# Optimization experiments

Hardware: AMD Instinct MI355X
Metric: run time of the kernel (lower is better)

The kernel has to match this reference:

```python
import jax, jax.numpy as jnp
import numpy as np


def setup_inputs() -> dict:
    key = jax.random.key(0)
    k1, k2 = jax.random.split(key)
    B, Sx, Sy, D = 8, 2048, 2048, 1024
    x = jax.random.normal(k1, (B, Sx, D), dtype=jnp.float32)
    y = jax.random.normal(k2, (B, Sy, D), dtype=jnp.float32)
    return {"x": x, "y": y}


def reference(x, y):
    # e[b,i,j] = x[b,i,:] . y[b,j,:]  (UNscaled, as in the original)
    e = jnp.einsum('bid,bjd->bij', x, y)
    ai = jax.nn.softmax(e, axis=-1)
    # a[b,i,:] = sum_j ai[b,i,j] * y[b,j,:]
    a = jnp.einsum('bij,bjd->bid', ai, y)
    # concat along feature dim; dropout p=0 -> identity
    out = jnp.concatenate([x, a], axis=-1)  # [B, Sx, 2D]
    return out
```

## Files before the change

### kernel.cpp

```cpp
#include <hip/hip_runtime.h>
#include <stdint.h>

#define SX 2048
#define SYY 2048
#define DDIM 1024
#define NBATCH 8

typedef _Float16 f16;
typedef __attribute__((ext_vector_type(2))) _Float16 h2_t;
typedef __attribute__((ext_vector_type(4))) _Float16 h4_t;
typedef __attribute__((ext_vector_type(8))) _Float16 h8_t;
typedef __attribute__((ext_vector_type(4))) float fx4_t;

__device__ __forceinline__ void gload_lds16(const void* g, void* l) {
  __builtin_amdgcn_global_load_lds((const __attribute__((address_space(1))) void*)g,
                                   (__attribute__((address_space(3))) void*)l,
                                   16, 0, 0);
}

__global__ __launch_bounds__(256) void k_prep_x(const float4* __restrict__ x,
                                                float* __restrict__ out,
                                                h4_t* __restrict__ x16, long n4) {
  long i = (long)blockIdx.x * blockDim.x + threadIdx.x;
  long stride = (long)gridDim.x * blockDim.x;
  for (; i < n4; i += stride) {
    long bi = i >> 8;
    int dq = (int)(i & 255);
    float4 v = x[i];
    *(float4*)(out + bi * (2 * DDIM) + dq * 4) = v;
    h4_t h = { (f16)v.x, (f16)v.y, (f16)v.z, (f16)v.w };
    x16[i] = h;
  }
}

__global__ __launch_bounds__(256) void k_trans(const float* __restrict__ y,
                                               f16* __restrict__ y16,
                                               f16* __restrict__ yt16) {
  __shared__ f16 tile[64][72];
  int z = blockIdx.z;
  int d0 = blockIdx.x * 64, j0 = blockIdx.y * 64;
  const float* yb = y + (size_t)z * SYY * DDIM;
  f16* y16b = y16 + (size_t)z * SYY * DDIM;
  f16* ytb = yt16 + (size_t)z * DDIM * SYY;
  int t = threadIdx.x;
  int jl = t >> 2;
  int dq = t & 3;
#pragma unroll
  for (int s = 0; s < 4; ++s) {
    int dl = dq * 16 + s * 4;
    float4 v = *(const float4*)(yb + (size_t)(j0 + jl) * DDIM + d0 + dl);
    h4_t h = { (f16)v.x, (f16)v.y, (f16)v.z, (f16)v.w };
    *(h4_t*)(y16b + (size_t)(j0 + jl) * DDIM + d0 + dl) = h;
    *(h4_t*)&tile[jl][dl] = h;
  }
  __syncthreads();
  int dl2 = t >> 2;
  int jq = t & 3;
  f16 vbuf[16] __attribute__((aligned(16)));
#pragma unroll
  for (int u = 0; u < 16; ++u) vbuf[u] = tile[jq * 16 + u][dl2];
  f16* orow = ytb + (size_t)(d0 + dl2) * SYY + j0 + jq * 16;
  *(uint4*)orow = *(const uint4*)&vbuf[0];
  *(uint4*)(orow + 8) = *(const uint4*)&vbuf[8];
}

#define PH_BAR() __builtin_amdgcn_s_barrier()

#define STAGE_A(SLOT, HALF, T) {                                               \
    const f16* s_ = aRow + (size_t)((HALF) * 64) * lda + (T) * 64;             \
    f16* d_ = lds + (SLOT) * 8192 + dstoff;                                    \
    gload_lds16(s_, d_);                                                       \
    gload_lds16(s_ + (size_t)128 * lda, d_ + 4096); }

#define STAGE_B(SLOT, HALF, T) {                                               \
    const f16* s_ = bRow + (size_t)((HALF) * 32) * ldb + (T) * 64;             \
    f16* d_ = lds + (SLOT) * 8192 + dstoff;                                    \
    gload_lds16(s_, d_);                                                       \
    gload_lds16(s_ + (size_t)128 * ldb, d_ + 4096); }

#define RD_A(PTR, CB) { _Pragma("unroll") for (int i_ = 0; i_ < 4; ++i_) {     \
    af[i_][0] = *(const h8_t*)((PTR) + (CB) + i_ * 2048 + kb0);                \
    af[i_][1] = *(const h8_t*)((PTR) + (CB) + i_ * 2048 + kb1); } }

#define RD_A_S(PTR, CB, MOFF) { _Pragma("unroll") for (int i_ = 0; i_ < 4; ++i_) { \
    h8_t a0 = *(const h8_t*)((PTR) + (CB) + i_ * 2048 + kb0);                  \
    h8_t a1 = *(const h8_t*)((PTR) + (CB) + i_ * 2048 + kb1);                  \
    h2_t* p0 = (h2_t*)&a0; h2_t* p1 = (h2_t*)&a1;                              \
    _Pragma("unroll") for (int q_ = 0; q_ < 4; ++q_) {                         \
      p0[q_] *= fdc[(MOFF) + i_]; p1[q_] *= fdc[(MOFF) + i_]; }                \
    af[i_][0] = a0; af[i_][1] = a1; } }

#define RD_B(PTR, CB, NH) { _Pragma("unroll") for (int j_ = 0; j_ < 2; ++j_) { \
    bf[(NH) + j_][0] = *(const h8_t*)((PTR) + (CB) + j_ * 2048 + kb0);         \
    bf[(NH) + j_][1] = *(const h8_t*)((PTR) + (CB) + j_ * 2048 + kb1); } }

#define MM(MH, NH) { __builtin_amdgcn_s_setprio(1);                            \
  _Pragma("unroll") for (int i_ = 0; i_ < 4; ++i_)                             \
  _Pragma("unroll") for (int j_ = 0; j_ < 2; ++j_) {                           \
    acc[(MH) + i_][(NH) + j_] = __builtin_amdgcn_mfma_f32_16x16x32_f16(        \
        af[i_][0], bf[(NH) + j_][0], acc[(MH) + i_][(NH) + j_], 0, 0, 0);      \
    acc[(MH) + i_][(NH) + j_] = __builtin_amdgcn_mfma_f32_16x16x32_f16(        \
        af[i_][1], bf[(NH) + j_][1], acc[(MH) + i_][(NH) + j_], 0, 0, 0); }    \
  __builtin_amdgcn_s_setprio(0); }

#define DECODE_TILE()                                                          \
  int bid = blockIdx.x;                                                        \
  int id = bid;                                                                \
  if ((nblk & 7) == 0) { int cpx = nblk >> 3; id = (bid & 7) * cpx + (bid >> 3); } \
  int tpz = ntm * ntn;                                                         \
  int z = id / tpz;                                                            \
  int rem = id - z * tpz;                                                      \
  int mt, ntl;                                                                 \
  if ((ntm & 1) == 0) {                                                        \
    int ht = tpz >> 1, hm = ntm >> 1;                                          \
    int half = rem / ht, j = rem - half * ht;                                  \
    ntl = j / hm; mt = half * hm + (j - ntl * hm);                             \
  } else { mt = rem / ntn; ntl = rem - mt * ntn; }                             \
  int m0 = mt * 256, n0 = ntl * 256;

#define GEMM_COMMON_SETUP()                                                    \
  const int tid = threadIdx.x;                                                 \
  const int lane = tid & 63, w = tid >> 6;                                     \
  const int wr = w >> 2, wc = w & 3;                                           \
  const int fr = lane & 15, fh = lane >> 4;                                    \
  const f16* Ab = A + (size_t)z * a_zs + (size_t)(a_row0 + m0) * lda;          \
  const f16* Bb = B + (size_t)z * b_zs + (size_t)n0 * ldb;                     \
  const int l0 = 8 * w + (lane >> 3);                                          \
  const int r0a = l0;                                                          \
  const int r0b = ((l0 >> 5) << 6) | (l0 & 31);                                \
  const int swz = 8 * ((lane & 7) ^ (lane >> 3));                              \
  const f16* aRow = Ab + (size_t)r0a * lda + swz;                              \
  const f16* bRow = Bb + (size_t)r0b * ldb + swz;                              \
  const int dstoff = w * 512 + lane * 8;                                       \
  const char* ldsAlo = (const char*)lds + wr * 8192 + fr * 128;                \
  const char* ldsAhi = ldsAlo + 16384;                                         \
  const char* ldsBlo = (const char*)lds + 32768 + wc * 4096 + fr * 128;        \
  const char* ldsBhi = ldsBlo + 16384;                                         \
  const int kb0 = ((0 + fh) ^ (fr & 7)) * 16;                                  \
  const int kb1 = ((4 + fh) ^ (fr & 7)) * 16;

__global__ __launch_bounds__(512, 2) void k_gemm1(
    const f16* __restrict__ A, long a_zs, int a_row0, int lda,
    const f16* __restrict__ B, long b_zs, int ldb,
    f16* __restrict__ U, long u_zs,
    float2* __restrict__ ML, int mrows,
    int K, int ntm, int ntn, int nblk)
{
  __shared__ f16 lds[65536];
  DECODE_TILE();
  GEMM_COMMON_SETUP();

  const int nt = K >> 6;
  const int ng = nt >> 1;

  fx4_t acc[8][4];
#pragma unroll
  for (int i = 0; i < 8; ++i)
#pragma unroll
    for (int j = 0; j < 4; ++j) { fx4_t zv = {0.f,0.f,0.f,0.f}; acc[i][j] = zv; }
  h8_t af[4][2], bf[4][2];

  STAGE_A(0, 0, 0); STAGE_A(1, 1, 0); STAGE_B(2, 0, 0); STAGE_B(3, 1, 0);
  STAGE_A(4, 0, 1); STAGE_B(6, 0, 1); STAGE_B(7, 1, 1);
  asm volatile("s_waitcnt vmcnt(6)" ::: "memory");
  PH_BAR();

  for (int g = 0; g < ng; ++g) {
    const int T1 = 2 * g + 1, T2 = 2 * g + 2, T3 = 2 * g + 3;
    const bool nl = (g < ng - 1);
    RD_A(ldsAlo, 0); RD_B(ldsBlo, 0, 0);
    STAGE_A(5, 1, T1);
    PH_BAR();
    MM(0, 0);
    PH_BAR();
    RD_B(ldsBhi, 0, 2);
    if (nl) STAGE_A(0, 0, T2);
    PH_BAR();
    MM(0, 2);
    PH_BAR();
    RD_A(ldsAhi, 0);
    if (nl) STAGE_B(2, 0, T2);
    PH_BAR();
    MM(4, 0);
    PH_BAR();
    if (nl) STAGE_B(3, 1, T2);
    PH_BAR();
    MM(4, 2);
    if (nl) { asm volatile("s_waitcnt vmcnt(6)" ::: "memory"); }
    else    { asm volatile("s_waitcnt vmcnt(0)" ::: "memory"); }
    PH_BAR();
    RD_A(ldsAlo, 65536); RD_B(ldsBlo, 65536, 0);
    if (nl) STAGE_A(1, 1, T2);
    PH_BAR();
    MM(0, 0);
    PH_BAR();
    RD_B(ldsBhi, 65536, 2);
    if (nl) STAGE_A(4, 0, T3);
    PH_BAR();
    MM(0, 2);
    PH_BAR();
    RD_A(ldsAhi, 65536);
    if (nl) STAGE_B(6, 0, T3);
    PH_BAR();
    MM(4, 0);
    PH_BAR();
    if (nl) STAGE_B(7, 1, T3);
    PH_BAR();
    MM(4, 2);
    asm volatile("s_waitcnt vmcnt(6)" ::: "memory");
    PH_BAR();
  }

  __syncthreads();
  float2* mlx = (float2*)lds;
  const int rbase = wr * 128 + fh * 4;
  float mw[8][4];
#pragma unroll
  for (int mi = 0; mi < 8; ++mi)
#pragma unroll
    for (int rr = 0; rr < 4; ++rr) {
      float am = fmaxf(fmaxf(acc[mi][0][rr], acc[mi][1][rr]),
                       fmaxf(acc[mi][2][rr], acc[mi][3][rr]));
      am = fmaxf(am, __shfl_xor(am, 1)); am = fmaxf(am, __shfl_xor(am, 2));
      am = fmaxf(am, __shfl_xor(am, 4)); am = fmaxf(am, __shfl_xor(am, 8));
      float s = 0.f;
#pragma unroll
      for (int ni = 0; ni < 4; ++ni) {
        float e = __expf(acc[mi][ni][rr] - am);
        acc[mi][ni][rr] = e; s += e;
      }
      s += __shfl_xor(s, 1); s += __shfl_xor(s, 2);
      s += __shfl_xor(s, 4); s += __shfl_xor(s, 8);
      mw[mi][rr] = am;
      if (fr == 0) {
        float2 v; v.x = am; v.y = s;
        mlx[(rbase + mi * 16 + rr) * 4 + wc] = v;
      }
    }
  __syncthreads();
  float2* MLp = ML + ((size_t)z * 8 + (n0 >> 8)) * mrows + m0;
#pragma unroll
  for (int mi = 0; mi < 8; ++mi)
#pragma unroll
    for (int rr = 0; rr < 4; ++rr) {
      int row = rbase + mi * 16 + rr;
      float4 p01 = *(float4*)&mlx[row * 4 + 0];
      float4 p23 = *(float4*)&mlx[row * 4 + 2];
      float mt = fmaxf(fmaxf(p01.x, p01.z), fmaxf(p23.x, p23.z));
      float lt = p01.y * __expf(p01.x - mt) + p01.w * __expf(p01.z - mt) +
                 p23.y * __expf(p23.x - mt) + p23.w * __expf(p23.z - mt);
      if (wc == 0 && fr == 0) { float2 v; v.x = mt; v.y = lt; MLp[row] = v; }
      mw[mi][rr] = __expf(mw[mi][rr] - mt);
    }
  __syncthreads();
  f16* wreg = lds + w * 8192;
#pragma unroll
  for (int mi = 0; mi < 8; ++mi)
#pragma unroll
    for (int ni = 0; ni < 4; ++ni)
#pragma unroll
      for (int rr = 0; rr < 4; ++rr)
        wreg[(mi * 16 + fh * 4 + rr) * 64 + ni * 16 + fr] =
            (f16)(acc[mi][ni][rr] * mw[mi][rr]);
  f16* Ub = U + (size_t)z * u_zs + (size_t)(m0 + wr * 128 + (lane >> 3)) * SYY +
            n0 + wc * 64 + (lane & 7) * 8;
  const f16* rsrc = wreg + (lane >> 3) * 64 + (lane & 7) * 8;
#pragma unroll
  for (int i = 0; i < 16; ++i)
    *(uint4*)(Ub + (size_t)(i * 8) * SYY) = *(const uint4*)(rsrc + i * 512);
}

__global__ __launch_bounds__(256) void k_mlred(const float2* __restrict__ ML,
                                               f16* __restrict__ Fq,
                                               int rows, long total) {
  long idx = (long)blockIdx.x * blockDim.x + threadIdx.x;
  if (idx >= total) return;
  int z = (int)(idx / rows);
  int r = (int)(idx - (long)z * rows);
  float2 v[8];
  float M = -3.4e38f;
#pragma unroll
  for (int t = 0; t < 8; ++t) {
    v[t] = ML[((size_t)z * 8 + t) * rows + r];
    M = fmaxf(M, v[t].x);
  }
  float L = 0.f;
#pragma unroll
  for (int t = 0; t < 8; ++t) L += v[t].y * __expf(v[t].x - M);
  float inv = 1.0f / L;
#pragma unroll
  for (int t = 0; t < 8; ++t)
    Fq[((size_t)z * 8 + t) * rows + r] = (f16)(__expf(v[t].x - M) * inv);
}

__global__ __launch_bounds__(512, 2) void k_gemm2(
    const f16* __restrict__ A, long a_zs, int a_row0, int lda,
    const f16* __restrict__ B, long b_zs, int ldb,
    float* __restrict__ C, long c_zs, int c_row0, int ldc, int c_col0,
    const f16* __restrict__ Fq, int mrows,
    int K, int ntm, int ntn, int nblk)
{
  __shared__ f16 lds[65536];
  DECODE_TILE();
  GEMM_COMMON_SETUP();

  const int nt = K >> 6;
  const int ng = nt >> 1;

  fx4_t acc[8][4];
#pragma unroll
  for (int i = 0; i < 8; ++i)
#pragma unroll
    for (int j = 0; j < 4; ++j) { fx4_t zv = {0.f,0.f,0.f,0.f}; acc[i][j] = zv; }
  h8_t af[4][2], bf[4][2];

  const f16* Fb = Fq + (size_t)z * 8 * mrows + m0 + wr * 128 + fr;
  h2_t fdc[8], fdn[8];
#pragma unroll
  for (int i = 0; i < 8; ++i) {
    f16 fv = Fb[i * 16];
    h2_t d; d[0] = fv; d[1] = fv; fdn[i] = d;
  }

  STAGE_A(0, 0, 0); STAGE_A(1, 1, 0); STAGE_B(2, 0, 0); STAGE_B(3, 1, 0);
  STAGE_A(4, 0, 1); STAGE_B(6, 0, 1); STAGE_B(7, 1, 1);
  asm volatile("s_waitcnt vmcnt(6)" ::: "memory");
  PH_BAR();

  for (int g = 0; g < ng; ++g) {
    const int T1 = 2 * g + 1, T2 = 2 * g + 2, T3 = 2 * g + 3;
    const bool nl = (g < ng - 1);
    const bool ev = ((g & 1) == 0);
    if (ev) {
#pragma unroll
      for (int i = 0; i < 8; ++i) fdc[i] = fdn[i];
    }
    RD_A_S(ldsAlo, 0, 0); RD_B(ldsBlo, 0, 0);
    STAGE_A(5, 1, T1);
    PH_BAR(); MM(0, 0); PH_BAR();
    RD_B(ldsBhi, 0, 2);
    if (nl) STAGE_A(0, 0, T2);
    PH_BAR(); MM(0, 2); PH_BAR();
    RD_A_S(ldsAhi, 0, 4);
    if (nl) STAGE_B(2, 0, T2);
    PH_BAR(); MM(4, 0); PH_BAR();
    if (nl) STAGE_B(3, 1, T2);
    PH_BAR(); MM(4, 2);
    if (nl) { asm volatile("s_waitcnt vmcnt(6)" ::: "memory"); }
    else    { asm volatile("s_waitcnt vmcnt(0)" ::: "memory"); }
    PH_BAR();
    RD_A_S(ldsAlo, 65536, 0); RD_B(ldsBlo, 65536, 0);
    if (ev) {
      int tn = (g >> 1) + 1;
      if (tn < 8) {
        const f16* Fn = Fb + (size_t)tn * mrows;
#pragma unroll
        for (int i = 0; i < 8; ++i) {
          f16 fv = Fn[i * 16];
          h2_t d; d[0] = fv; d[1] = fv; fdn[i] = d;
        }
      }
    }
    if (nl) STAGE_A(1, 1, T2);
    PH_BAR(); MM(0, 0); PH_BAR();
    RD_B(ldsBhi, 65536, 2);
    if (nl) STAGE_A(4, 0, T3);
    PH_BAR(); MM(0, 2); PH_BAR();
    RD_A_S(ldsAhi, 65536, 4);
    if (nl) STAGE_B(6, 0, T3);
    PH_BAR(); MM(4, 0); PH_BAR();
    if (nl) STAGE_B(7, 1, T3);
    PH_BAR(); MM(4, 2);
    asm volatile("s_waitcnt vmcnt(6)" ::: "memory");
    PH_BAR();
  }

  float* Cb = C + (size_t)z * c_zs +
              (size_t)(c_row0 + m0 + wr * 128) * ldc + c_col0 + n0 + wc * 64;
#pragma unroll
  for (int mi = 0; mi < 8; ++mi)
#pragma unroll
    for (int ni = 0; ni < 4; ++ni)
#pragma unroll
      for (int r = 0; r < 4; ++r)
        Cb[(size_t)(mi * 16 + fh * 4 + r) * ldc + ni * 16 + fr] = acc[mi][ni][r];
}

extern "C" void kernel_launch(void* const* d_in, const int* in_sizes, int n_in,
                              void* d_out, int out_size, void* d_ws, size_t ws_size,
                              hipStream_t stream) {
  (void)in_sizes; (void)n_in; (void)out_size;
  const float* x = (const float*)d_in[0];
  const float* y = (const float*)d_in[1];
  float* out = (float*)d_out;

  size_t per_batch = (size_t)SX * SYY * 2 + (size_t)8 * SX * 8 + (size_t)8 * SX * 2 +
                     (size_t)SX * DDIM * 2 + (size_t)SYY * DDIM * 2 +
                     (size_t)DDIM * SYY * 2;
  int nb = (int)(ws_size / per_batch);
  if (nb > NBATCH) nb = NBATCH;
  int CH = SX;
  if (nb < 1) {
    nb = 1;
    size_t conv = (size_t)SX * DDIM * 2 + (size_t)SYY * DDIM * 2 +
                  (size_t)DDIM * SYY * 2;
    size_t avail = ws_size > conv ? ws_size - conv : 0;
    long ch = (long)(avail / ((size_t)SYY * 2 + 80));
    ch = (ch / 256) * 256;
    if (ch < 256) ch = 256;
    if (ch > SX) ch = SX;
    CH = (int)ch;
  }

  char* w = (char*)d_ws;
  f16* Ubuf = (f16*)w;            size_t off = (size_t)nb * CH * SYY * 2;
  float2* MLbuf = (float2*)(w + off); off += (size_t)nb * 8 * CH * 8;
  f16* Fqbuf = (f16*)(w + off);   off += (size_t)nb * 8 * CH * 2;
  f16* X16 = (f16*)(w + off);     off += (size_t)nb * SX * DDIM * 2;
  f16* Y16 = (f16*)(w + off);     off += (size_t)nb * SYY * DDIM * 2;
  f16* Yt16 = (f16*)(w + off);

  for (int b0 = 0; b0 < NBATCH; b0 += nb) {
    int nbc = (NBATCH - b0 < nb) ? (NBATCH - b0) : nb;
    k_prep_x<<<2048, 256, 0, stream>>>(
        (const float4*)(x + (size_t)b0 * SX * DDIM),
        out + (size_t)b0 * SX * 2 * DDIM, (h4_t*)X16,
        (long)nbc * SX * (DDIM / 4));
    dim3 tg(DDIM / 64, SYY / 64, nbc);
    k_trans<<<tg, 256, 0, stream>>>(y + (size_t)b0 * SYY * DDIM, Y16, Yt16);

    for (int i0 = 0; i0 < SX; i0 += CH) {
      int ntm = CH / 256;
      int nblk1 = nbc * ntm * (SYY / 256);
      k_gemm1<<<nblk1, 512, 0, stream>>>(X16, (long)SX * DDIM, i0, DDIM,
                                         Y16, (long)SYY * DDIM, DDIM,
                                         Ubuf, (long)CH * SYY,
                                         MLbuf, CH,
                                         DDIM, ntm, SYY / 256, nblk1);
      long rows_total = (long)nbc * CH;
      k_mlred<<<(unsigned)((rows_total + 255) / 256), 256, 0, stream>>>(
          MLbuf, Fqbuf, CH, rows_total);
      int nblk2 = nbc * ntm * (DDIM / 256);
      k_gemm2<<<nblk2, 512, 0, stream>>>(Ubuf, (long)CH * SYY, 0, SYY,
                                         Yt16, (long)DDIM * SYY, SYY,
                                         out + (size_t)b0 * SX * 2 * DDIM,
                                         (long)SX * 2 * DDIM, i0, 2 * DDIM, DDIM,
                                         Fqbuf, CH,
                                         SYY, ntm, DDIM / 256, nblk2);
    }
  }
}
```

Baseline: 231.3 us.

## Drop in-block softmax stat merge; emit per-wave partials and scale per 64 columns

The gemm1 epilogue no longer merges row max/sum across the four column waves through LDS with two block barriers. Each wave now writes its own 64-column partial (max, sum) and stores its unscaled exponentials straight to global memory. The reduction kernel merges 32 partials per row instead of 8, and gemm2 switches scale factors every 64-wide K chunk, loading two factor sets per iteration. This removes barriers and LDS staging, at the cost of uncoalesced 2-byte global stores in place of 16-byte vector stores, plus more reduction and factor-load work.

```diff
diff --git a/kernel.cpp b/kernel.cpp
--- a/kernel.cpp
+++ b/kernel.cpp
@@ -82,12 +82,12 @@
     af[i_][0] = *(const h8_t*)((PTR) + (CB) + i_ * 2048 + kb0);                \
     af[i_][1] = *(const h8_t*)((PTR) + (CB) + i_ * 2048 + kb1); } }
 
-#define RD_A_S(PTR, CB, MOFF) { _Pragma("unroll") for (int i_ = 0; i_ < 4; ++i_) { \
+#define RD_A_S(PTR, CB, MOFF, FD) { _Pragma("unroll") for (int i_ = 0; i_ < 4; ++i_) { \
     h8_t a0 = *(const h8_t*)((PTR) + (CB) + i_ * 2048 + kb0);                  \
     h8_t a1 = *(const h8_t*)((PTR) + (CB) + i_ * 2048 + kb1);                  \
     h2_t* p0 = (h2_t*)&a0; h2_t* p1 = (h2_t*)&a1;                              \
     _Pragma("unroll") for (int q_ = 0; q_ < 4; ++q_) {                         \
-      p0[q_] *= fdc[(MOFF) + i_]; p1[q_] *= fdc[(MOFF) + i_]; }                \
+      p0[q_] *= FD[(MOFF) + i_]; p1[q_] *= FD[(MOFF) + i_]; }                  \
     af[i_][0] = a0; af[i_][1] = a1; } }
 
 #define RD_B(PTR, CB, NH) { _Pragma("unroll") for (int j_ = 0; j_ < 2; ++j_) { \
@@ -211,10 +211,9 @@
     PH_BAR();
   }
 
-  __syncthreads();
-  float2* mlx = (float2*)lds;
   const int rbase = wr * 128 + fh * 4;
-  float mw[8][4];
+  f16* Ub = U + (size_t)z * u_zs;
+  float2* MLp = ML + (((size_t)z * 8 + (n0 >> 8)) * 4 + wc) * mrows + m0;
 #pragma unroll
   for (int mi = 0; mi < 8; ++mi)
 #pragma unroll
@@ -231,43 +230,13 @@
       }
       s += __shfl_xor(s, 1); s += __shfl_xor(s, 2);
       s += __shfl_xor(s, 4); s += __shfl_xor(s, 8);
-      mw[mi][rr] = am;
-      if (fr == 0) {
-        float2 v; v.x = am; v.y = s;
-        mlx[(rbase + mi * 16 + rr) * 4 + wc] = v;
-      }
+      int row = rbase + mi * 16 + rr;
+      if (fr == 0) { float2 v; v.x = am; v.y = s; MLp[row] = v; }
+#pragma unroll
+      for (int ni = 0; ni < 4; ++ni)
+        Ub[(size_t)(m0 + row) * SYY + n0 + wc * 64 + ni * 16 + fr] =
+            (f16)acc[mi][ni][rr];
     }
-  __syncthreads();
-  float2* MLp = ML + ((size_t)z * 8 + (n0 >> 8)) * mrows + m0;
-#pragma unroll
-  for (int mi = 0; mi < 8; ++mi)
-#pragma unroll
-    for (int rr = 0; rr < 4; ++rr) {
-      int row = rbase + mi * 16 + rr;
-      float4 p01 = *(float4*)&mlx[row * 4 + 0];
-      float4 p23 = *(float4*)&mlx[row * 4 + 2];
-      float mt = fmaxf(fmaxf(p01.x, p01.z), fmaxf(p23.x, p23.z));
-      float lt = p01.y * __expf(p01.x - mt) + p01.w * __expf(p01.z - mt) +
-                 p23.y * __expf(p23.x - mt) + p23.w * __expf(p23.z - mt);
-      if (wc == 0 && fr == 0) { float2 v; v.x = mt; v.y = lt; MLp[row] = v; }
-      mw[mi][rr] = __expf(mw[mi][rr] - mt);
-    }
-  __syncthreads();
-  f16* wreg = lds + w * 8192;
-#pragma unroll
-  for (int mi = 0; mi < 8; ++mi)
-#pragma unroll
-    for (int ni = 0; ni < 4; ++ni)
-#pragma unroll
-      for (int rr = 0; rr < 4; ++rr)
-        wreg[(mi * 16 + fh * 4 + rr) * 64 + ni * 16 + fr] =
-            (f16)(acc[mi][ni][rr] * mw[mi][rr]);
-  f16* Ub = U + (size_t)z * u_zs + (size_t)(m0 + wr * 128 + (lane >> 3)) * SYY +
-            n0 + wc * 64 + (lane & 7) * 8;
-  const f16* rsrc = wreg + (lane >> 3) * 64 + (lane & 7) * 8;
-#pragma unroll
-  for (int i = 0; i < 16; ++i)
-    *(uint4*)(Ub + (size_t)(i * 8) * SYY) = *(const uint4*)(rsrc + i * 512);
 }
 
 __global__ __launch_bounds__(256) void k_mlred(const float2* __restrict__ ML,
@@ -277,20 +246,20 @@
   if (idx >= total) return;
   int z = (int)(idx / rows);
   int r = (int)(idx - (long)z * rows);
-  float2 v[8];
   float M = -3.4e38f;
-#pragma unroll
-  for (int t = 0; t < 8; ++t) {
-    v[t] = ML[((size_t)z * 8 + t) * rows + r];
+  float2 v[32];
+#pragma unroll
+  for (int t = 0; t < 32; ++t) {
+    v[t] = ML[((size_t)z * 32 + t) * rows + r];
     M = fmaxf(M, v[t].x);
   }
   float L = 0.f;
 #pragma unroll
-  for (int t = 0; t < 8; ++t) L += v[t].y * __expf(v[t].x - M);
+  for (int t = 0; t < 32; ++t) L += v[t].y * __expf(v[t].x - M);
   float inv = 1.0f / L;
 #pragma unroll
-  for (int t = 0; t < 8; ++t)
-    Fq[((size_t)z * 8 + t) * rows + r] = (f16)(__expf(v[t].x - M) * inv);
+  for (int t = 0; t < 32; ++t)
+    Fq[((size_t)z * 32 + t) * rows + r] = (f16)(__expf(v[t].x - M) * inv);
 }
 
 __global__ __launch_bounds__(512, 2) void k_gemm2(
@@ -314,12 +283,13 @@
     for (int j = 0; j < 4; ++j) { fx4_t zv = {0.f,0.f,0.f,0.f}; acc[i][j] = zv; }
   h8_t af[4][2], bf[4][2];
 
-  const f16* Fb = Fq + (size_t)z * 8 * mrows + m0 + wr * 128 + fr;
-  h2_t fdc[8], fdn[8];
+  const f16* Fb = Fq + (size_t)z * 32 * mrows + m0 + wr * 128 + fr;
+  h2_t fcA[8], fcB[8], fnA[8], fnB[8];
 #pragma unroll
   for (int i = 0; i < 8; ++i) {
-    f16 fv = Fb[i * 16];
-    h2_t d; d[0] = fv; d[1] = fv; fdn[i] = d;
+    f16 a = Fb[i * 16], b = Fb[(size_t)mrows + i * 16];
+    h2_t da; da[0] = a; da[1] = a; fnA[i] = da;
+    h2_t db; db[0] = b; db[1] = b; fnB[i] = db;
   }
 
   STAGE_A(0, 0, 0); STAGE_A(1, 1, 0); STAGE_B(2, 0, 0); STAGE_B(3, 1, 0);
@@ -330,18 +300,15 @@
   for (int g = 0; g < ng; ++g) {
     const int T1 = 2 * g + 1, T2 = 2 * g + 2, T3 = 2 * g + 3;
     const bool nl = (g < ng - 1);
-    const bool ev = ((g & 1) == 0);
-    if (ev) {
-#pragma unroll
-      for (int i = 0; i < 8; ++i) fdc[i] = fdn[i];
-    }
-    RD_A_S(ldsAlo, 0, 0); RD_B(ldsBlo, 0, 0);
+#pragma unroll
+    for (int i = 0; i < 8; ++i) { fcA[i] = fnA[i]; fcB[i] = fnB[i]; }
+    RD_A_S(ldsAlo, 0, 0, fcA); RD_B(ldsBlo, 0, 0);
     STAGE_A(5, 1, T1);
     PH_BAR(); MM(0, 0); PH_BAR();
     RD_B(ldsBhi, 0, 2);
     if (nl) STAGE_A(0, 0, T2);
     PH_BAR(); MM(0, 2); PH_BAR();
-    RD_A_S(ldsAhi, 0, 4);
+    RD_A_S(ldsAhi, 0, 4, fcA);
     if (nl) STAGE_B(2, 0, T2);
     PH_BAR(); MM(4, 0); PH_BAR();
     if (nl) STAGE_B(3, 1, T2);
@@ -349,16 +316,14 @@
     if (nl) { asm volatile("s_waitcnt vmcnt(6)" ::: "memory"); }
     else    { asm volatile("s_waitcnt vmcnt(0)" ::: "memory"); }
     PH_BAR();
-    RD_A_S(ldsAlo, 65536, 0); RD_B(ldsBlo, 65536, 0);
-    if (ev) {
-      int tn = (g >> 1) + 1;
-      if (tn < 8) {
-        const f16* Fn = Fb + (size_t)tn * mrows;
-#pragma unroll
-        for (int i = 0; i < 8; ++i) {
-          f16 fv = Fn[i * 16];
-          h2_t d; d[0] = fv; d[1] = fv; fdn[i] = d;
-        }
+    RD_A_S(ldsAlo, 65536, 0, fcB); RD_B(ldsBlo, 65536, 0);
+    if (nl) {
+      const f16* Fn = Fb + (size_t)(2 * g + 2) * mrows;
+#pragma unroll
+      for (int i = 0; i < 8; ++i) {
+        f16 a = Fn[i * 16], b = Fn[(size_t)mrows + i * 16];
+        h2_t da; da[0] = a; da[1] = a; fnA[i] = da;
+        h2_t db; db[0] = b; db[1] = b; fnB[i] = db;
       }
     }
     if (nl) STAGE_A(1, 1, T2);
@@ -366,7 +331,7 @@
     RD_B(ldsBhi, 65536, 2);
     if (nl) STAGE_A(4, 0, T3);
     PH_BAR(); MM(0, 2); PH_BAR();
-    RD_A_S(ldsAhi, 65536, 4);
+    RD_A_S(ldsAhi, 65536, 4, fcB);
     if (nl) STAGE_B(6, 0, T3);
     PH_BAR(); MM(4, 0); PH_BAR();
     if (nl) STAGE_B(7, 1, T3);
@@ -394,7 +359,7 @@
   const float* y = (const float*)d_in[1];
   float* out = (float*)d_out;
 
-  size_t per_batch = (size_t)SX * SYY * 2 + (size_t)8 * SX * 8 + (size_t)8 * SX * 2 +
+  size_t per_batch = (size_t)SX * SYY * 2 + (size_t)32 * SX * 8 + (size_t)32 * SX * 2 +
                      (size_t)SX * DDIM * 2 + (size_t)SYY * DDIM * 2 +
                      (size_t)DDIM * SYY * 2;
   int nb = (int)(ws_size / per_batch);
@@ -405,7 +370,7 @@
     size_t conv = (size_t)SX * DDIM * 2 + (size_t)SYY * DDIM * 2 +
                   (size_t)DDIM * SYY * 2;
     size_t avail = ws_size > conv ? ws_size - conv : 0;
-    long ch = (long)(avail / ((size_t)SYY * 2 + 80));
+    long ch = (long)(avail / ((size_t)SYY * 2 + 320));
     ch = (ch / 256) * 256;
     if (ch < 256) ch = 256;
     if (ch > SX) ch = SX;
@@ -414,8 +379,8 @@
 
   char* w = (char*)d_ws;
   f16* Ubuf = (f16*)w;            size_t off = (size_t)nb * CH * SYY * 2;
-  float2* MLbuf = (float2*)(w + off); off += (size_t)nb * 8 * CH * 8;
-  f16* Fqbuf = (f16*)(w + off);   off += (size_t)nb * 8 * CH * 2;
+  float2* MLbuf = (float2*)(w + off); off += (size_t)nb * 32 * CH * 8;
+  f16* Fqbuf = (f16*)(w + off);   off += (size_t)nb * 32 * CH * 2;
   f16* X16 = (f16*)(w + off);     off += (size_t)nb * SX * DDIM * 2;
   f16* Y16 = (f16*)(w + off);     off += (size_t)nb * SYY * DDIM * 2;
   f16* Yt16 = (f16*)(w + off);
```

Result: slower. 262.9 us (+13.7%).
